# Kernel optimization log

Hardware: AMD Instinct MI355X
Metric: run time of the kernel (lower is better)

Reference implementation:

```python
import jax, jax.numpy as jnp
import numpy as np

CATS = [1000, 1000, 2000]
NDS = len(CATS)
TOT = sum(CATS)          # total_cats = 4000
N = TOT + NDS            # 4003 source (label) nodes
U = 2048                 # num_unify_class
NFEAT = 256
F = 256                  # nfeat_out
OUT_FEAT = 512           # output_feat_dim
ADJ_FEAT = 256           # adj_feat_dim
SINKHORN_ITERS = 20


def setup_inputs() -> dict:
    key = jax.random.key(0)
    ks = jax.random.split(key, 16)

    def rn(k, shape, s):
        return jax.random.normal(k, shape, dtype=jnp.float32) * s

    return {
        "datasets_node_features": jax.random.normal(ks[0], (TOT, NFEAT), dtype=jnp.float32),
        "unlable_node_features": rn(ks[1], (NDS, NFEAT), 0.02),  # trunc_normal_(std=0.02)
        "adj_matrix": jax.random.uniform(ks[2], (N, U), dtype=jnp.float32),  # torch.rand init
        "W_before": rn(ks[3], (NFEAT, F), 0.05), "b_before": jnp.zeros((F,), jnp.float32),
        "gc1_W": rn(ks[4], (F, F), 0.05), "gc1_b": jnp.zeros((F,), jnp.float32),
        "gc2_W": rn(ks[5], (F, F), 0.05), "gc2_b": jnp.zeros((F,), jnp.float32),
        "gc3_W": rn(ks[6], (F, F), 0.05), "gc3_b": jnp.zeros((F,), jnp.float32),
        "W1": rn(ks[7], (F, OUT_FEAT), 0.05), "b1": jnp.zeros((OUT_FEAT,), jnp.float32),
        "W2": rn(ks[8], (OUT_FEAT, ADJ_FEAT), 0.05), "b2": jnp.zeros((ADJ_FEAT,), jnp.float32),
    }


def _log_optimal_transport(scores, iters):
    # log-space Sinkhorn with uniform marginals 1/(m+n), then rescale by (m+n)
    m, n = scores.shape
    norm = -jnp.log(jnp.asarray(m + n, scores.dtype))
    log_mu = jnp.full((m,), norm, scores.dtype)
    log_nu = jnp.full((n,), norm, scores.dtype)

    def body(carry, _):
        u, v = carry
        u = log_mu - jax.nn.logsumexp(scores + v[None, :], axis=1)
        v = log_nu - jax.nn.logsumexp(scores + u[:, None], axis=0)
        return (u, v), None

    (u, v), _ = jax.lax.scan(body, (jnp.zeros_like(log_mu), jnp.zeros_like(log_nu)),
                             None, length=iters)
    return scores + u[:, None] + v[None, :] - norm


def reference(datasets_node_features, unlable_node_features, adj_matrix,
              W_before, b_before, gc1_W, gc1_b, gc2_W, gc2_b, gc3_W, gc3_b,
              W1, b1, W2, b2):
    # node features: dataset class nodes + per-dataset 'unlabeled' nodes -> [N, NFEAT]
    feats = jnp.concatenate([datasets_node_features, unlable_node_features], axis=0)
    x = jax.nn.relu(feats @ W_before + b_before)  # [N, F]

    # learnable adjacency normalized via differentiable Sinkhorn OT  [N, U]
    A = jnp.exp(_log_optimal_transport(adj_matrix, SINKHORN_ITERS))

    # bipartite message passing: full graph adj has zero diagonal blocks,
    # so spmm(adj, h) splits into A @ h_u (into label nodes) and A.T @ h_n (into unify nodes).
    hn = x                 # [N, F] label-node features
    hu = A.T @ x           # [U, F] initial unify-node features via aggregation

    def gcn(hn, hu, W, b):
        # GraphConvolution: spmm(adj, h @ W) + b ; GCN wrapper: tanh(out + h)
        new_n = jnp.tanh(A @ (hu @ W) + b + hn)
        new_u = jnp.tanh(A.T @ (hn @ W) + b + hu)
        return new_n, new_u

    hn, hu = gcn(hn, hu, gc1_W, gc1_b)
    hn, hu = gcn(hn, hu, gc2_W, gc2_b)
    hn, hu = gcn(hn, hu, gc3_W, gc3_b)

    # output head on unify nodes: linear1 -> relu -> linear2  [U, ADJ_FEAT]
    out = jax.nn.relu(hu @ W1 + b1) @ W2 + b2
    return out
```

## Files before the change

### kernel.cpp

```cpp
#include <hip/hip_runtime.h>
#include <hip/hip_fp16.h>
#include <math.h>

#define NN 4003
#define UU 2048
#define KP 4032
#define N4P 4004
#define NORMC (-8.7079796f)

using bf16x8 = __attribute__((ext_vector_type(8))) short;
using f32x4  = __attribute__((ext_vector_type(4))) float;

#define GLL16(g, l) __builtin_amdgcn_global_load_lds( \
    (const __attribute__((address_space(1))) unsigned*)(g), \
    (__attribute__((address_space(3))) unsigned*)(l), 16, 0, 0)

__device__ __forceinline__ ushort f2bf(float x) {
    unsigned u = __builtin_bit_cast(unsigned, x);
    u += 0x7fff + ((u >> 16) & 1);
    return (ushort)(u >> 16);
}
__device__ __forceinline__ float bf2f(ushort h) {
    unsigned u = ((unsigned)h) << 16;
    return __builtin_bit_cast(float, u);
}
__device__ __forceinline__ void bfsplit(float x, ushort& hi, ushort& lo) {
    hi = f2bf(x);
    lo = f2bf(x - bf2f(hi));
}
__device__ __forceinline__ float h2f(ushort h) {
    return __half2float(__ushort_as_half(h));
}

__global__ void concat_bf(const float* __restrict__ a, const float* __restrict__ b,
                          ushort* __restrict__ fh, ushort* __restrict__ fl,
                          float* __restrict__ u_ext, float* __restrict__ v) {
    int bid = blockIdx.x;
    if (bid >= 1001) {
        if (bid < 1003) {
            int t = (bid - 1001) * 256 + threadIdx.x;
            if (t < 512) ((float4*)v)[t] = (float4){0.f, 0.f, 0.f, 0.f};
        } else {
            if ((int)threadIdx.x < KP - NN) u_ext[NN + threadIdx.x] = -1e30f;
        }
        return;
    }
    int i = bid * 256 + threadIdx.x;
    const int tot4 = NN * 256 / 4;
    if (i >= tot4) return;
    float4 vv = (i < 256000) ? ((const float4*)a)[i] : ((const float4*)b)[i - 256000];
    ushort4 hv, lv;
    bfsplit(vv.x, hv.x, lv.x); bfsplit(vv.y, hv.y, lv.y);
    bfsplit(vv.z, hv.z, lv.z); bfsplit(vv.w, hv.w, lv.w);
    *(ushort4*)(fh + ((size_t)i << 2)) = hv;
    *(ushort4*)(fl + ((size_t)i << 2)) = lv;
}

__global__ void convW_all(
        const float* __restrict__ Wa, const float* __restrict__ Wb_,
        const float* __restrict__ Wc, const float* __restrict__ Wd,
        const float* __restrict__ We, const float* __restrict__ Wf,
        ushort* T0h, ushort* T0l, ushort* T1h, ushort* T1l,
        ushort* T2h, ushort* T2l, ushort* T3h, ushort* T3l,
        ushort* T4h, ushort* T4l, ushort* T5h, ushort* T5l) {
    __shared__ float tile[32][33];
    const float* W; ushort* Th; ushort* Tl; int K, Nw;
    switch (blockIdx.z) {
        case 0:  W = Wa;  Th = T0h; Tl = T0l; K = 256; Nw = 256; break;
        case 1:  W = Wb_; Th = T1h; Tl = T1l; K = 256; Nw = 256; break;
        case 2:  W = Wc;  Th = T2h; Tl = T2l; K = 256; Nw = 256; break;
        case 3:  W = Wd;  Th = T3h; Tl = T3l; K = 256; Nw = 256; break;
        case 4:  W = We;  Th = T4h; Tl = T4l; K = 256; Nw = 512; break;
        default: W = Wf;  Th = T5h; Tl = T5l; K = 512; Nw = 256; break;
    }
    int bx = blockIdx.x, by = blockIdx.y;
    if (bx * 32 >= Nw || by * 32 >= K) return;
    int tx = threadIdx.x;
    for (int r = threadIdx.y; r < 32; r += 8)
        tile[r][tx] = W[(size_t)(by * 32 + r) * Nw + bx * 32 + tx];
    __syncthreads();
    for (int r = threadIdx.y; r < 32; r += 8) {
        int n = bx * 32 + r, k = by * 32 + tx;
        ushort hi, lo; bfsplit(tile[tx][r], hi, lo);
        Th[(size_t)n * K + k] = hi;
        Tl[(size_t)n * K + k] = lo;
    }
}

__global__ void conv_both(const float* __restrict__ in, ushort* __restrict__ Sh,
                          ushort* __restrict__ STh) {
    __shared__ float tile[32][33];
    int x = blockIdx.x * 32 + threadIdx.x;
    int y0 = blockIdx.y * 32;
    for (int r = threadIdx.y; r < 32; r += 8) {
        int y = y0 + r;
        float vv = (y < NN) ? in[(size_t)y * UU + x] : 0.0f;
        tile[r][threadIdx.x] = vv;
        if (y < NN)
            Sh[(size_t)y * UU + x] = __half_as_ushort(__float2half(vv));
    }
    __syncthreads();
    int oc = y0 + threadIdx.x;
    for (int r = threadIdx.y; r < 32; r += 8) {
        int orow = blockIdx.x * 32 + r;
        STh[(size_t)orow * KP + oc] = __half_as_ushort(__float2half(tile[threadIdx.x][r]));
    }
}

__device__ __forceinline__ void wave_lse_reduce(float& m, float& s) {
    #pragma unroll
    for (int off = 1; off < 64; off <<= 1) {
        float om = __shfl_xor(m, off, 64), os = __shfl_xor(s, off, 64);
        float nm = fmaxf(m, om);
        s = s * __expf(m - nm) + os * __expf(om - nm);
        m = nm;
    }
}

__global__ __launch_bounds__(256) void lse4h(const ushort* __restrict__ Sh, int lda,
                                             const float* __restrict__ addv,
                                             float* __restrict__ outv, int C, int R) {
    int r0 = blockIdx.x * 4;
    const ushort* rp[4];
    #pragma unroll
    for (int q = 0; q < 4; ++q) {
        int r = r0 + q; if (r >= R) r = R - 1;
        rp[q] = Sh + (size_t)r * lda;
    }
    float m[4], s[4];
    #pragma unroll
    for (int q = 0; q < 4; ++q) { m[q] = -INFINITY; s[q] = 0.0f; }
    int C4 = C >> 2;
    for (int j = threadIdx.x; j < C4; j += 256) {
        float4 av = ((const float4*)addv)[j];
        #pragma unroll
        for (int q = 0; q < 4; ++q) {
            ushort4 pa = *(const ushort4*)(rp[q] + (j << 2));
            float x0 = h2f(pa.x) + av.x, x1 = h2f(pa.y) + av.y;
            float x2 = h2f(pa.z) + av.z, x3 = h2f(pa.w) + av.w;
            float mx = fmaxf(fmaxf(x0, x1), fmaxf(x2, x3));
            float nm = fmaxf(m[q], mx);
            s[q] = s[q] * __expf(m[q] - nm) + __expf(x0 - nm) + __expf(x1 - nm)
                                            + __expf(x2 - nm) + __expf(x3 - nm);
            m[q] = nm;
        }
    }
    int rem = C & 3;
    if ((int)threadIdx.x < rem) {
        int j = (C4 << 2) + threadIdx.x;
        float av = addv[j];
        #pragma unroll
        for (int q = 0; q < 4; ++q) {
            float x = h2f(rp[q][j]) + av;
            float nm = fmaxf(m[q], x);
            s[q] = s[q] * __expf(m[q] - nm) + __expf(x - nm);
            m[q] = nm;
        }
    }
    #pragma unroll
    for (int q = 0; q < 4; ++q) wave_lse_reduce(m[q], s[q]);
    __shared__ float sm[4][4], ss[4][4];
    int w = threadIdx.x >> 6;
    if ((threadIdx.x & 63) == 0) {
        #pragma unroll
        for (int q = 0; q < 4; ++q) { sm[w][q] = m[q]; ss[w][q] = s[q]; }
    }
    __syncthreads();
    if (threadIdx.x < 4) {
        int q = threadIdx.x;
        float mm = sm[0][q], sa = ss[0][q];
        #pragma unroll
        for (int i = 1; i < 4; ++i) {
            float om = sm[i][q], os = ss[i][q];
            float nm = fmaxf(mm, om);
            sa = sa * __expf(mm - nm) + os * __expf(om - nm);
            mm = nm;
        }
        int r = r0 + q;
        if (r < R) outv[r] = NORMC - (mm + __logf(sa));
    }
}

__device__ __forceinline__ void exp_row8h(const ushort* __restrict__ Sh,
        const float* __restrict__ rowadd, const float* __restrict__ coladd,
        int lda, int M, int gm, int kbase, uint4& hiv, uint4& lov) {
    ushort h[8], l[8];
    if (gm < M) {
        float ra = rowadd[gm] - NORMC;
        const ushort* rp = Sh + (size_t)gm * lda + kbase;
        ushort4 q0 = *(const ushort4*)rp;
        ushort4 q1 = *(const ushort4*)(rp + 4);
        float4 ca = *(const float4*)(coladd + kbase);
        float4 cb = *(const float4*)(coladd + kbase + 4);
        float vv[8] = {h2f(q0.x) + ca.x, h2f(q0.y) + ca.y, h2f(q0.z) + ca.z, h2f(q0.w) + ca.w,
                       h2f(q1.x) + cb.x, h2f(q1.y) + cb.y, h2f(q1.z) + cb.z, h2f(q1.w) + cb.w};
        #pragma unroll
        for (int e = 0; e < 8; ++e) {
            float av = __expf(vv[e] + ra);
            bfsplit(av, h[e], l[e]);
        }
    } else {
        #pragma unroll
        for (int e = 0; e < 8; ++e) { h[e] = 0; l[e] = 0; }
    }
    hiv.x = (unsigned)h[0] | ((unsigned)h[1] << 16);
    hiv.y = (unsigned)h[2] | ((unsigned)h[3] << 16);
    hiv.z = (unsigned)h[4] | ((unsigned)h[5] << 16);
    hiv.w = (unsigned)h[6] | ((unsigned)h[7] << 16);
    lov.x = (unsigned)l[0] | ((unsigned)l[1] << 16);
    lov.y = (unsigned)l[2] | ((unsigned)l[3] << 16);
    lov.z = (unsigned)l[4] | ((unsigned)l[5] << 16);
    lov.w = (unsigned)l[6] | ((unsigned)l[7] << 16);
}

__global__ __launch_bounds__(512) __attribute__((amdgpu_waves_per_eu(2, 4)))
void gemm_bigN(
        const ushort* __restrict__ Sh, const float* __restrict__ rowadd,
        const float* __restrict__ coladd, int lda,
        const ushort* __restrict__ Bh, const ushort* __restrict__ Bl, int ldb,
        float* __restrict__ P, int M, int K, int Kc) {
    __shared__ __align__(16) ushort SM[2 * 64 * 64 + 2 * 256 * 64];
    ushort* As0 = SM;
    ushort* As1 = SM + 4096;
    ushort* Bs0 = SM + 8192;
    ushort* Bs1 = SM + 8192 + 16384;
    const int tid = threadIdx.x;
    const int bm = blockIdx.x << 6;
    const int lane = tid & 63;
    const int wv = tid >> 6;
    const int wr = (wv >> 2) << 5;
    const int wc = (wv & 3) << 6;
    const int kb = blockIdx.y * Kc;
    int ke = kb + Kc; if (ke > K) ke = K;
    const int arow = tid >> 3, ak8 = (tid & 7) << 3;
    const int as = ((arow << 6) + ak8) ^ ((arow & 7) << 3);
    const int brow_base = wv << 5;
    f32x4 acc[2][4] = {};
    for (int k0 = kb; k0 < ke; k0 += 64) {
        uint4 ah, al;
        exp_row8h(Sh, rowadd, coladd, lda, M, bm + arow, k0 + ak8, ah, al);
        __syncthreads();
        #pragma unroll
        for (int t = 0; t < 4; ++t) {
            int rb2 = brow_base + (t << 3);
            int row = rb2 + (lane >> 3);
            int kksrc = (((lane & 7) ^ (row & 7)) << 3);
            size_t go = (size_t)row * ldb + k0 + kksrc;
            GLL16(Bh + go, &Bs0[rb2 << 6]);
            GLL16(Bl + go, &Bs1[rb2 << 6]);
        }
        *(uint4*)&As0[as] = ah;
        *(uint4*)&As1[as] = al;
        __syncthreads();
        #pragma unroll
        for (int ks = 0; ks < 2; ++ks) {
            int kq = (ks << 5) + ((lane >> 4) << 3);
            bf16x8 fah[2], fal[2], fbh[4], fbl[4];
            #pragma unroll
            for (int f = 0; f < 2; ++f) {
                int rr = wr + (f << 4) + (lane & 15);
                int ia = ((rr << 6) + kq) ^ ((rr & 7) << 3);
                fah[f] = *(const bf16x8*)&As0[ia];
                fal[f] = *(const bf16x8*)&As1[ia];
            }
            #pragma unroll
            for (int g = 0; g < 4; ++g) {
                int cc = wc + (g << 4) + (lane & 15);
                int ib = ((cc << 6) + kq) ^ ((cc & 7) << 3);
                fbh[g] = *(const bf16x8*)&Bs0[ib];
                fbl[g] = *(const bf16x8*)&Bs1[ib];
            }
            #pragma unroll
            for (int i = 0; i < 2; ++i)
                #pragma unroll
                for (int j = 0; j < 4; ++j) {
                    acc[i][j] = __builtin_amdgcn_mfma_f32_16x16x32_bf16(fah[i], fbh[j], acc[i][j], 0, 0, 0);
                    acc[i][j] = __builtin_amdgcn_mfma_f32_16x16x32_bf16(fah[i], fbl[j], acc[i][j], 0, 0, 0);
                    acc[i][j] = __builtin_amdgcn_mfma_f32_16x16x32_bf16(fal[i], fbh[j], acc[i][j], 0, 0, 0);
                }
        }
    }
    __syncthreads();
    float* LF = (float*)SM;
    #pragma unroll
    for (int i = 0; i < 2; ++i) {
        int row0 = wr + (i << 4) + ((lane >> 4) << 2);
        #pragma unroll
        for (int j = 0; j < 4; ++j) {
            int col = wc + (j << 4) + (lane & 15);
            #pragma unroll
            for (int r = 0; r < 4; ++r)
                LF[(row0 + r) * 256 + col] = acc[i][j][r];
        }
    }
    __syncthreads();
    float* Pp = P + (size_t)blockIdx.y * ((size_t)M * 256);
    #pragma unroll
    for (int it = 0; it < 8; ++it) {
        int idx = tid + (it << 9);
        int row = idx >> 6, c4 = (idx & 63) << 2;
        if (bm + row < M)
            *(float4*)(Pp + (size_t)(bm + row) * 256 + c4) = *(const float4*)&LF[row * 256 + c4];
    }
}

__global__ __launch_bounds__(256) __attribute__((amdgpu_waves_per_eu(4, 8)))
void gemm_ks(
        const ushort* __restrict__ Ah, const ushort* __restrict__ Al, int lda,
        const ushort* __restrict__ Bh, const ushort* __restrict__ Bl, int ldb, int Nb,
        float* __restrict__ P, int M, int Nplane, int K, int Kc) {
    __shared__ __align__(16) ushort SM[4 * 64 * 64];
    ushort* As0 = SM;
    ushort* As1 = SM + 4096;
    ushort* Bs0 = SM + 8192;
    ushort* Bs1 = SM + 12288;
    const int tid = threadIdx.x;
    const int bm = blockIdx.y << 6, bn = blockIdx.x << 6;
    const int lane = tid & 63;
    const int wv = tid >> 6;
    const int wm = (wv >> 1) << 5, wn = (wv & 1) << 5;
    const int kb = blockIdx.z * Kc;
    int ke = kb + Kc; if (ke > K) ke = K;
    const int rb = wv << 4;
    f32x4 acc[2][2] = {};
    for (int k0 = kb; k0 < ke; k0 += 64) {
        __syncthreads();
        #pragma unroll
        for (int t = 0; t < 2; ++t) {
            int rb2 = rb + (t << 3);
            int row = rb2 + (lane >> 3);
            int kksrc = (((lane & 7) ^ (row & 7)) << 3);
            int ga = bm + row; ga = (ga < M) ? ga : (M - 1);
            int gb = bn + row; gb = (gb < Nb) ? gb : (Nb - 1);
            size_t goa = (size_t)ga * lda + k0 + kksrc;
            size_t gob = (size_t)gb * ldb + k0 + kksrc;
            GLL16(Ah + goa, &As0[rb2 << 6]);
            GLL16(Al + goa, &As1[rb2 << 6]);
            GLL16(Bh + gob, &Bs0[rb2 << 6]);
            GLL16(Bl + gob, &Bs1[rb2 << 6]);
        }
        __syncthreads();
        #pragma unroll
        for (int ks = 0; ks < 2; ++ks) {
            int kbq = (ks << 5) + ((lane >> 4) << 3);
            bf16x8 fah[2], fal[2], fbh[2], fbl[2];
            #pragma unroll
            for (int f = 0; f < 2; ++f) {
                int rr = wm + (f << 4) + (lane & 15);
                int ia = ((rr << 6) + kbq) ^ ((rr & 7) << 3);
                fah[f] = *(const bf16x8*)&As0[ia];
                fal[f] = *(const bf16x8*)&As1[ia];
                int cc = wn + (f << 4) + (lane & 15);
                int ib = ((cc << 6) + kbq) ^ ((cc & 7) << 3);
                fbh[f] = *(const bf16x8*)&Bs0[ib];
                fbl[f] = *(const bf16x8*)&Bs1[ib];
            }
            #pragma unroll
            for (int i = 0; i < 2; ++i)
                #pragma unroll
                for (int j = 0; j < 2; ++j) {
                    acc[i][j] = __builtin_amdgcn_mfma_f32_16x16x32_bf16(fah[i], fbh[j], acc[i][j], 0, 0, 0);
                    acc[i][j] = __builtin_amdgcn_mfma_f32_16x16x32_bf16(fah[i], fbl[j], acc[i][j], 0, 0, 0);
                    acc[i][j] = __builtin_amdgcn_mfma_f32_16x16x32_bf16(fal[i], fbh[j], acc[i][j], 0, 0, 0);
                }
        }
    }
    __syncthreads();
    float* LF = (float*)SM;
    #pragma unroll
    for (int i = 0; i < 2; ++i) {
        int row0 = wm + (i << 4) + ((lane >> 4) << 2);
        #pragma unroll
        for (int j = 0; j < 2; ++j) {
            int col = wn + (j << 4) + (lane & 15);
            #pragma unroll
            for (int r = 0; r < 4; ++r)
                LF[(row0 + r) * 64 + col] = acc[i][j][r];
        }
    }
    __syncthreads();
    float* Pp = P + (size_t)blockIdx.z * ((size_t)M * Nplane);
    #pragma unroll
    for (int it = 0; it < 4; ++it) {
        int idx = tid + (it << 8);
        int row = idx >> 4, c4 = (idx & 15) << 2;
        if (bm + row < M && bn + c4 < Nplane)
            *(float4*)(Pp + (size_t)(bm + row) * Nplane + bn + c4) = *(const float4*)&LF[row * 64 + c4];
    }
}

template<int ACT, int BIAS, int RES, int OUTK>
__global__ __launch_bounds__(256) void reduce_ks(
        const float* __restrict__ P, int zg,
        const float* __restrict__ bias,
        const ushort* __restrict__ Rh, const ushort* __restrict__ Rl,
        float* __restrict__ Cf, ushort* __restrict__ Ch, ushort* __restrict__ Cl,
        int M, int N4, int ldo) {
    int t = blockIdx.x * 256 + threadIdx.x;
    int n4w = N4 >> 2;
    int tot = M * n4w;
    if (t >= tot) return;
    int m = t / n4w;
    int n = (t - m * n4w) << 2;
    size_t pstr = (size_t)M * N4;
    const float* base = P + (size_t)m * N4 + n;
    float4 a = *(const float4*)base;
    for (int z = 1; z < zg; ++z) {
        float4 b = *(const float4*)(base + (size_t)z * pstr);
        a.x += b.x; a.y += b.y; a.z += b.z; a.w += b.w;
    }
    if (BIAS == 1) {
        float4 bv = *(const float4*)(bias + n);
        a.x += bv.x; a.y += bv.y; a.z += bv.z; a.w += bv.w;
    }
    if (BIAS == 2) {
        float s = bias[m];
        a.x += s; a.y += s; a.z += s; a.w += s;
    }
    if (RES) {
        size_t ro = (size_t)m * ldo + n;
        ushort4 rh = *(const ushort4*)(Rh + ro);
        ushort4 rl = *(const ushort4*)(Rl + ro);
        a.x += bf2f(rh.x) + bf2f(rl.x); a.y += bf2f(rh.y) + bf2f(rl.y);
        a.z += bf2f(rh.z) + bf2f(rl.z); a.w += bf2f(rh.w) + bf2f(rl.w);
    }
    if (ACT == 1) {
        a.x = fmaxf(a.x, 0.f); a.y = fmaxf(a.y, 0.f);
        a.z = fmaxf(a.z, 0.f); a.w = fmaxf(a.w, 0.f);
    }
    if (ACT == 2) {
        a.x = tanhf(a.x); a.y = tanhf(a.y); a.z = tanhf(a.z); a.w = tanhf(a.w);
    }
    size_t co = (size_t)m * ldo + n;
    if (OUTK == 0) {
        *(float4*)(Cf + co) = a;
    } else {
        ushort4 hv, lv;
        bfsplit(a.x, hv.x, lv.x); bfsplit(a.y, hv.y, lv.y);
        bfsplit(a.z, hv.z, lv.z); bfsplit(a.w, hv.w, lv.w);
        *(ushort4*)(Ch + co) = hv;
        *(ushort4*)(Cl + co) = lv;
    }
}

static inline int rgrid(int M, int N4) { return (M * (N4 >> 2) + 255) / 256; }

extern "C" void kernel_launch(void* const* d_in, const int* in_sizes, int n_in,
                              void* d_out, int out_size, void* d_ws, size_t ws_size,
                              hipStream_t stream) {
    const float* dsf = (const float*)d_in[0];
    const float* unl = (const float*)d_in[1];
    const float* S   = (const float*)d_in[2];
    const float* Wb  = (const float*)d_in[3];
    const float* bb  = (const float*)d_in[4];
    const float* gcW[3] = {(const float*)d_in[5], (const float*)d_in[7], (const float*)d_in[9]};
    const float* gcb[3] = {(const float*)d_in[6], (const float*)d_in[8], (const float*)d_in[10]};
    const float* W1 = (const float*)d_in[11];
    const float* b1 = (const float*)d_in[12];
    const float* W2 = (const float*)d_in[13];
    const float* b2 = (const float*)d_in[14];
    float* out = (float*)d_out;

    char* p = (char*)d_ws;
    ushort* Shm = (ushort*)p; p += (size_t)NN * UU * 2;
    ushort* STh = (ushort*)p; p += (size_t)UU * KP * 2;
    float* P    = (float*)p;  p += (size_t)8 * NN * 256 * 4;
    ushort* fh = (ushort*)p; ushort* fl = fh + (size_t)NN * 256; p += (size_t)NN * 256 * 4;
    ushort* xh = (ushort*)p; ushort* xl = xh + (size_t)NN * 256; p += (size_t)NN * 256 * 4;
    ushort* xTh = (ushort*)p; ushort* xTl = xTh + (size_t)256 * KP; p += (size_t)256 * KP * 4;
    ushort* huh = (ushort*)p; ushort* hul = huh + (size_t)UU * 256; p += (size_t)UU * 256 * 4;
    ushort* tuTh = (ushort*)p; ushort* tuTl = tuTh + (size_t)256 * UU; p += (size_t)256 * UU * 4;
    ushort* tnTh = (ushort*)p; ushort* tnTl = tnTh + (size_t)256 * KP; p += (size_t)256 * KP * 4;
    float* u_ext = (float*)p; p += KP * 4;
    float* v     = (float*)p; p += UU * 4;
    ushort* WbTh = (ushort*)p; ushort* WbTl = WbTh + 256 * 256; p += 256 * 256 * 4;
    ushort* gWh[3]; ushort* gWl[3];
    for (int l = 0; l < 3; ++l) { gWh[l] = (ushort*)p; gWl[l] = gWh[l] + 256 * 256; p += 256 * 256 * 4; }
    ushort* W1Th = (ushort*)p; ushort* W1Tl = W1Th + 512 * 256; p += 512 * 256 * 4;
    ushort* W2Th = (ushort*)p; ushort* W2Tl = W2Th + 256 * 512; p += 256 * 512 * 4;
    ushort* h1h = xh; ushort* h1l = h1h + (size_t)UU * 512;
    (void)ws_size;

    concat_bf<<<dim3(1004), dim3(256), 0, stream>>>(dsf, unl, fh, fl, u_ext, v);
    convW_all<<<dim3(16, 16, 6), dim3(32, 8), 0, stream>>>(
        Wb, gcW[0], gcW[1], gcW[2], W1, W2,
        WbTh, WbTl, gWh[0], gWl[0], gWh[1], gWl[1], gWh[2], gWl[2],
        W1Th, W1Tl, W2Th, W2Tl);
    conv_both<<<dim3(64, 126), dim3(32, 8), 0, stream>>>(S, Shm, STh);

    gemm_ks<<<dim3(4, 63, 2), 256, 0, stream>>>(
        fh, fl, 256, WbTh, WbTl, 256, 256, P, NN, 256, 256, 128);
    reduce_ks<1,1,0,1><<<rgrid(NN,256), 256, 0, stream>>>(
        P, 2, bb, nullptr, nullptr, nullptr, xh, xl, NN, 256, 256);
    gemm_ks<<<dim3(63, 4, 2), 256, 0, stream>>>(
        WbTh, WbTl, 256, fh, fl, 256, NN, P, 256, N4P, 256, 128);
    reduce_ks<1,2,0,1><<<rgrid(256,N4P), 256, 0, stream>>>(
        P, 2, bb, nullptr, nullptr, nullptr, xTh, xTl, 256, N4P, KP);

    for (int it = 0; it < 20; ++it) {
        lse4h<<<dim3((NN + 3) / 4), dim3(256), 0, stream>>>(Shm, UU, v, u_ext, UU, NN);
        lse4h<<<dim3(UU / 4),       dim3(256), 0, stream>>>(STh, KP, u_ext, v, NN, UU);
    }

    gemm_bigN<<<dim3(32, 8), 512, 0, stream>>>(
        STh, v, u_ext, KP, xTh, xTl, KP, P, UU, KP, 512);
    reduce_ks<0,0,0,1><<<rgrid(UU,256), 256, 0, stream>>>(
        P, 8, nullptr, nullptr, nullptr, nullptr, huh, hul, UU, 256, 256);

    for (int l = 0; l < 3; ++l) {
        const ushort* hnh = (l == 0) ? xh : fh;
        const ushort* hnl = (l == 0) ? xl : fl;
        if (l < 2) {
            gemm_ks<<<dim3(32, 4, 2), 256, 0, stream>>>(
                gWh[l], gWl[l], 256, huh, hul, 256, UU, P, 256, UU, 256, 128);
            reduce_ks<0,0,0,1><<<rgrid(256,UU), 256, 0, stream>>>(
                P, 2, nullptr, nullptr, nullptr, nullptr, tuTh, tuTl, 256, UU, UU);
        }
        gemm_ks<<<dim3(63, 4, 2), 256, 0, stream>>>(
            gWh[l], gWl[l], 256, hnh, hnl, 256, NN, P, 256, N4P, 256, 128);
        reduce_ks<0,0,0,1><<<rgrid(256,N4P), 256, 0, stream>>>(
            P, 2, nullptr, nullptr, nullptr, nullptr, tnTh, tnTl, 256, N4P, KP);
        if (l < 2) {
            gemm_bigN<<<dim3(63, 6), 512, 0, stream>>>(
                Shm, u_ext, v, UU, tuTh, tuTl, UU, P, NN, UU, 384);
            reduce_ks<2,1,1,1><<<rgrid(NN,256), 256, 0, stream>>>(
                P, 6, gcb[l], hnh, hnl, nullptr, fh, fl, NN, 256, 256);
        }
        gemm_bigN<<<dim3(32, 8), 512, 0, stream>>>(
            STh, v, u_ext, KP, tnTh, tnTl, KP, P, UU, KP, 512);
        reduce_ks<2,1,1,1><<<rgrid(UU,256), 256, 0, stream>>>(
            P, 8, gcb[l], huh, hul, nullptr, huh, hul, UU, 256, 256);
    }

    gemm_ks<<<dim3(8, 32, 2), 256, 0, stream>>>(
        huh, hul, 256, W1Th, W1Tl, 256, 512, P, UU, 512, 256, 128);
    reduce_ks<1,1,0,1><<<rgrid(UU,512), 256, 0, stream>>>(
        P, 2, b1, nullptr, nullptr, nullptr, h1h, h1l, UU, 512, 512);
    gemm_ks<<<dim3(4, 32, 4), 256, 0, stream>>>(
        h1h, h1l, 512, W2Th, W2Tl, 512, 256, P, UU, 256, 512, 128);
    reduce_ks<0,1,0,0><<<rgrid(UU,256), 256, 0, stream>>>(
        P, 4, b2, nullptr, nullptr, out, nullptr, nullptr, UU, 256, 256);
}
```

Before: 560.2 us.

## Fuse split-K reductions into GEMM kernels via last-block atomic counters

Removes the separate reduce_ks launches. Each split-K GEMM block now writes its partial tile, fences, and bumps a per-tile atomic counter. The last block for a tile sums all partials and applies bias, residual, activation and the bf16 hi/lo split itself. Counters are zeroed in concat_bf. This cuts about 14 kernel launches and their gaps, at the cost of atomics, fences and one serial reduction block per tile.

```diff
diff --git a/kernel.cpp b/kernel.cpp
--- a/kernel.cpp
+++ b/kernel.cpp
@@ -34,14 +34,18 @@
 
 __global__ void concat_bf(const float* __restrict__ a, const float* __restrict__ b,
                           ushort* __restrict__ fh, ushort* __restrict__ fl,
-                          float* __restrict__ u_ext, float* __restrict__ v) {
+                          float* __restrict__ u_ext, float* __restrict__ v,
+                          int* __restrict__ ctr) {
     int bid = blockIdx.x;
     if (bid >= 1001) {
         if (bid < 1003) {
             int t = (bid - 1001) * 256 + threadIdx.x;
             if (t < 512) ((float4*)v)[t] = (float4){0.f, 0.f, 0.f, 0.f};
+        } else if (bid == 1003) {
+            if ((int)threadIdx.x < KP - NN) u_ext[NN + threadIdx.x] = -1e30f;
         } else {
-            if ((int)threadIdx.x < KP - NN) u_ext[NN + threadIdx.x] = -1e30f;
+            int t = (bid - 1004) * 256 + threadIdx.x;
+            if (t < 960) ((int4*)ctr)[t] = (int4){0, 0, 0, 0};
         }
         return;
     }
@@ -213,12 +217,17 @@
     lov.w = (unsigned)l[6] | ((unsigned)l[7] << 16);
 }
 
+template<int ACT, int BIAS, int RES>
 __global__ __launch_bounds__(512) __attribute__((amdgpu_waves_per_eu(2, 4)))
 void gemm_bigN(
         const ushort* __restrict__ Sh, const float* __restrict__ rowadd,
         const float* __restrict__ coladd, int lda,
         const ushort* __restrict__ Bh, const ushort* __restrict__ Bl, int ldb,
-        float* __restrict__ P, int M, int K, int Kc) {
+        float* __restrict__ P, int M, int K, int Kc,
+        const float* __restrict__ bias,
+        const ushort* __restrict__ Rh, const ushort* __restrict__ Rl,
+        ushort* __restrict__ Ch, ushort* __restrict__ Cl,
+        int* __restrict__ ctr) {
     __shared__ __align__(16) ushort SM[2 * 64 * 64 + 2 * 256 * 64];
     ushort* As0 = SM;
     ushort* As1 = SM + 4096;
@@ -302,13 +311,58 @@
         if (bm + row < M)
             *(float4*)(Pp + (size_t)(bm + row) * 256 + c4) = *(const float4*)&LF[row * 256 + c4];
     }
-}
-
+    __threadfence();
+    __shared__ int lastf;
+    if (tid == 0) lastf = (atomicAdd(ctr + blockIdx.x, 1) == (int)gridDim.y - 1);
+    __syncthreads();
+    if (!lastf) return;
+    __threadfence();
+    const int zg = gridDim.y;
+    const size_t pstr = (size_t)M * 256;
+    #pragma unroll
+    for (int it = 0; it < 8; ++it) {
+        int idx = tid + (it << 9);
+        int row = idx >> 6, c4 = (idx & 63) << 2;
+        int grow = bm + row;
+        if (grow >= M) continue;
+        const float* base = P + (size_t)grow * 256 + c4;
+        float4 a = *(const float4*)base;
+        for (int z = 1; z < zg; ++z) {
+            float4 b2 = *(const float4*)(base + (size_t)z * pstr);
+            a.x += b2.x; a.y += b2.y; a.z += b2.z; a.w += b2.w;
+        }
+        if (BIAS == 1) {
+            float4 bv = *(const float4*)(bias + c4);
+            a.x += bv.x; a.y += bv.y; a.z += bv.z; a.w += bv.w;
+        }
+        if (RES) {
+            size_t ro = (size_t)grow * 256 + c4;
+            ushort4 rh = *(const ushort4*)(Rh + ro);
+            ushort4 rl = *(const ushort4*)(Rl + ro);
+            a.x += bf2f(rh.x) + bf2f(rl.x); a.y += bf2f(rh.y) + bf2f(rl.y);
+            a.z += bf2f(rh.z) + bf2f(rl.z); a.w += bf2f(rh.w) + bf2f(rl.w);
+        }
+        if (ACT == 2) {
+            a.x = tanhf(a.x); a.y = tanhf(a.y); a.z = tanhf(a.z); a.w = tanhf(a.w);
+        }
+        ushort4 hv, lv;
+        bfsplit(a.x, hv.x, lv.x); bfsplit(a.y, hv.y, lv.y);
+        bfsplit(a.z, hv.z, lv.z); bfsplit(a.w, hv.w, lv.w);
+        size_t co = (size_t)grow * 256 + c4;
+        *(ushort4*)(Ch + co) = hv;
+        *(ushort4*)(Cl + co) = lv;
+    }
+}
+
+template<int ACT, int BIAS, int OUTF>
 __global__ __launch_bounds__(256) __attribute__((amdgpu_waves_per_eu(4, 8)))
 void gemm_ks(
         const ushort* __restrict__ Ah, const ushort* __restrict__ Al, int lda,
         const ushort* __restrict__ Bh, const ushort* __restrict__ Bl, int ldb, int Nb,
-        float* __restrict__ P, int M, int Nplane, int K, int Kc) {
+        float* __restrict__ P, int M, int Nplane, int K, int Kc,
+        const float* __restrict__ bias,
+        float* __restrict__ Cf, ushort* __restrict__ Ch, ushort* __restrict__ Cl,
+        int ldo, int* __restrict__ ctr) {
     __shared__ __align__(16) ushort SM[4 * 64 * 64];
     ushort* As0 = SM;
     ushort* As1 = SM + 4096;
@@ -387,63 +441,51 @@
         if (bm + row < M && bn + c4 < Nplane)
             *(float4*)(Pp + (size_t)(bm + row) * Nplane + bn + c4) = *(const float4*)&LF[row * 64 + c4];
     }
-}
-
-template<int ACT, int BIAS, int RES, int OUTK>
-__global__ __launch_bounds__(256) void reduce_ks(
-        const float* __restrict__ P, int zg,
-        const float* __restrict__ bias,
-        const ushort* __restrict__ Rh, const ushort* __restrict__ Rl,
-        float* __restrict__ Cf, ushort* __restrict__ Ch, ushort* __restrict__ Cl,
-        int M, int N4, int ldo) {
-    int t = blockIdx.x * 256 + threadIdx.x;
-    int n4w = N4 >> 2;
-    int tot = M * n4w;
-    if (t >= tot) return;
-    int m = t / n4w;
-    int n = (t - m * n4w) << 2;
-    size_t pstr = (size_t)M * N4;
-    const float* base = P + (size_t)m * N4 + n;
-    float4 a = *(const float4*)base;
-    for (int z = 1; z < zg; ++z) {
-        float4 b = *(const float4*)(base + (size_t)z * pstr);
-        a.x += b.x; a.y += b.y; a.z += b.z; a.w += b.w;
-    }
-    if (BIAS == 1) {
-        float4 bv = *(const float4*)(bias + n);
-        a.x += bv.x; a.y += bv.y; a.z += bv.z; a.w += bv.w;
-    }
-    if (BIAS == 2) {
-        float s = bias[m];
-        a.x += s; a.y += s; a.z += s; a.w += s;
-    }
-    if (RES) {
-        size_t ro = (size_t)m * ldo + n;
-        ushort4 rh = *(const ushort4*)(Rh + ro);
-        ushort4 rl = *(const ushort4*)(Rl + ro);
-        a.x += bf2f(rh.x) + bf2f(rl.x); a.y += bf2f(rh.y) + bf2f(rl.y);
-        a.z += bf2f(rh.z) + bf2f(rl.z); a.w += bf2f(rh.w) + bf2f(rl.w);
-    }
-    if (ACT == 1) {
-        a.x = fmaxf(a.x, 0.f); a.y = fmaxf(a.y, 0.f);
-        a.z = fmaxf(a.z, 0.f); a.w = fmaxf(a.w, 0.f);
-    }
-    if (ACT == 2) {
-        a.x = tanhf(a.x); a.y = tanhf(a.y); a.z = tanhf(a.z); a.w = tanhf(a.w);
-    }
-    size_t co = (size_t)m * ldo + n;
-    if (OUTK == 0) {
-        *(float4*)(Cf + co) = a;
-    } else {
-        ushort4 hv, lv;
-        bfsplit(a.x, hv.x, lv.x); bfsplit(a.y, hv.y, lv.y);
-        bfsplit(a.z, hv.z, lv.z); bfsplit(a.w, hv.w, lv.w);
-        *(ushort4*)(Ch + co) = hv;
-        *(ushort4*)(Cl + co) = lv;
-    }
-}
-
-static inline int rgrid(int M, int N4) { return (M * (N4 >> 2) + 255) / 256; }
+    __threadfence();
+    __shared__ int lastf;
+    if (tid == 0)
+        lastf = (atomicAdd(ctr + blockIdx.y * gridDim.x + blockIdx.x, 1) == (int)gridDim.z - 1);
+    __syncthreads();
+    if (!lastf) return;
+    __threadfence();
+    const int zg = gridDim.z;
+    const size_t pstr = (size_t)M * Nplane;
+    #pragma unroll
+    for (int it = 0; it < 16; ++it) {
+        int idx = tid + (it << 8);
+        int row = idx >> 4, c4 = (idx & 15) << 2;
+        int grow = bm + row, gcol = bn + c4;
+        if (grow >= M || gcol >= Nplane) continue;
+        const float* base = P + (size_t)grow * Nplane + gcol;
+        float4 a = *(const float4*)base;
+        for (int z = 1; z < zg; ++z) {
+            float4 b2 = *(const float4*)(base + (size_t)z * pstr);
+            a.x += b2.x; a.y += b2.y; a.z += b2.z; a.w += b2.w;
+        }
+        if (BIAS == 1) {
+            float4 bv = *(const float4*)(bias + gcol);
+            a.x += bv.x; a.y += bv.y; a.z += bv.z; a.w += bv.w;
+        }
+        if (BIAS == 2) {
+            float sb = bias[grow];
+            a.x += sb; a.y += sb; a.z += sb; a.w += sb;
+        }
+        if (ACT == 1) {
+            a.x = fmaxf(a.x, 0.f); a.y = fmaxf(a.y, 0.f);
+            a.z = fmaxf(a.z, 0.f); a.w = fmaxf(a.w, 0.f);
+        }
+        size_t co = (size_t)grow * ldo + gcol;
+        if (OUTF) {
+            *(float4*)(Cf + co) = a;
+        } else {
+            ushort4 hv, lv;
+            bfsplit(a.x, hv.x, lv.x); bfsplit(a.y, hv.y, lv.y);
+            bfsplit(a.z, hv.z, lv.z); bfsplit(a.w, hv.w, lv.w);
+            *(ushort4*)(Ch + co) = hv;
+            *(ushort4*)(Cl + co) = lv;
+        }
+    }
+}
 
 extern "C" void kernel_launch(void* const* d_in, const int* in_sizes, int n_in,
                               void* d_out, int out_size, void* d_ws, size_t ws_size,
@@ -478,66 +520,59 @@
     for (int l = 0; l < 3; ++l) { gWh[l] = (ushort*)p; gWl[l] = gWh[l] + 256 * 256; p += 256 * 256 * 4; }
     ushort* W1Th = (ushort*)p; ushort* W1Tl = W1Th + 512 * 256; p += 512 * 256 * 4;
     ushort* W2Th = (ushort*)p; ushort* W2Tl = W2Th + 256 * 512; p += 256 * 512 * 4;
+    int* CTR = (int*)p; p += 15 * 256 * 4;
     ushort* h1h = xh; ushort* h1l = h1h + (size_t)UU * 512;
     (void)ws_size;
-
-    concat_bf<<<dim3(1004), dim3(256), 0, stream>>>(dsf, unl, fh, fl, u_ext, v);
+    int ci = 0;
+
+    concat_bf<<<dim3(1008), dim3(256), 0, stream>>>(dsf, unl, fh, fl, u_ext, v, CTR);
     convW_all<<<dim3(16, 16, 6), dim3(32, 8), 0, stream>>>(
         Wb, gcW[0], gcW[1], gcW[2], W1, W2,
         WbTh, WbTl, gWh[0], gWl[0], gWh[1], gWl[1], gWh[2], gWl[2],
         W1Th, W1Tl, W2Th, W2Tl);
     conv_both<<<dim3(64, 126), dim3(32, 8), 0, stream>>>(S, Shm, STh);
 
-    gemm_ks<<<dim3(4, 63, 2), 256, 0, stream>>>(
-        fh, fl, 256, WbTh, WbTl, 256, 256, P, NN, 256, 256, 128);
-    reduce_ks<1,1,0,1><<<rgrid(NN,256), 256, 0, stream>>>(
-        P, 2, bb, nullptr, nullptr, nullptr, xh, xl, NN, 256, 256);
-    gemm_ks<<<dim3(63, 4, 2), 256, 0, stream>>>(
-        WbTh, WbTl, 256, fh, fl, 256, NN, P, 256, N4P, 256, 128);
-    reduce_ks<1,2,0,1><<<rgrid(256,N4P), 256, 0, stream>>>(
-        P, 2, bb, nullptr, nullptr, nullptr, xTh, xTl, 256, N4P, KP);
+    gemm_ks<1,1,0><<<dim3(4, 63, 2), 256, 0, stream>>>(
+        fh, fl, 256, WbTh, WbTl, 256, 256, P, NN, 256, 256, 128,
+        bb, nullptr, xh, xl, 256, CTR + 256 * ci); ci++;
+    gemm_ks<1,2,0><<<dim3(63, 4, 2), 256, 0, stream>>>(
+        WbTh, WbTl, 256, fh, fl, 256, NN, P, 256, N4P, 256, 128,
+        bb, nullptr, xTh, xTl, KP, CTR + 256 * ci); ci++;
 
     for (int it = 0; it < 20; ++it) {
         lse4h<<<dim3((NN + 3) / 4), dim3(256), 0, stream>>>(Shm, UU, v, u_ext, UU, NN);
         lse4h<<<dim3(UU / 4),       dim3(256), 0, stream>>>(STh, KP, u_ext, v, NN, UU);
     }
 
-    gemm_bigN<<<dim3(32, 8), 512, 0, stream>>>(
-        STh, v, u_ext, KP, xTh, xTl, KP, P, UU, KP, 512);
-    reduce_ks<0,0,0,1><<<rgrid(UU,256), 256, 0, stream>>>(
-        P, 8, nullptr, nullptr, nullptr, nullptr, huh, hul, UU, 256, 256);
+    gemm_bigN<0,0,0><<<dim3(32, 8), 512, 0, stream>>>(
+        STh, v, u_ext, KP, xTh, xTl, KP, P, UU, KP, 512,
+        nullptr, nullptr, nullptr, huh, hul, CTR + 256 * ci); ci++;
 
     for (int l = 0; l < 3; ++l) {
         const ushort* hnh = (l == 0) ? xh : fh;
         const ushort* hnl = (l == 0) ? xl : fl;
         if (l < 2) {
-            gemm_ks<<<dim3(32, 4, 2), 256, 0, stream>>>(
-                gWh[l], gWl[l], 256, huh, hul, 256, UU, P, 256, UU, 256, 128);
-            reduce_ks<0,0,0,1><<<rgrid(256,UU), 256, 0, stream>>>(
-                P, 2, nullptr, nullptr, nullptr, nullptr, tuTh, tuTl, 256, UU, UU);
-        }
-        gemm_ks<<<dim3(63, 4, 2), 256, 0, stream>>>(
-            gWh[l], gWl[l], 256, hnh, hnl, 256, NN, P, 256, N4P, 256, 128);
-        reduce_ks<0,0,0,1><<<rgrid(256,N4P), 256, 0, stream>>>(
-            P, 2, nullptr, nullptr, nullptr, nullptr, tnTh, tnTl, 256, N4P, KP);
+            gemm_ks<0,0,0><<<dim3(32, 4, 2), 256, 0, stream>>>(
+                gWh[l], gWl[l], 256, huh, hul, 256, UU, P, 256, UU, 256, 128,
+                nullptr, nullptr, tuTh, tuTl, UU, CTR + 256 * ci); ci++;
+        }
+        gemm_ks<0,0,0><<<dim3(63, 4, 2), 256, 0, stream>>>(
+            gWh[l], gWl[l], 256, hnh, hnl, 256, NN, P, 256, N4P, 256, 128,
+            nullptr, nullptr, tnTh, tnTl, KP, CTR + 256 * ci); ci++;
         if (l < 2) {
-            gemm_bigN<<<dim3(63, 6), 512, 0, stream>>>(
-                Shm, u_ext, v, UU, tuTh, tuTl, UU, P, NN, UU, 384);
-            reduce_ks<2,1,1,1><<<rgrid(NN,256), 256, 0, stream>>>(
-                P, 6, gcb[l], hnh, hnl, nullptr, fh, fl, NN, 256, 256);
-        }
-        gemm_bigN<<<dim3(32, 8), 512, 0, stream>>>(
-            STh, v, u_ext, KP, tnTh, tnTl, KP, P, UU, KP, 512);
-        reduce_ks<2,1,1,1><<<rgrid(UU,256), 256, 0, stream>>>(
-            P, 8, gcb[l], huh, hul, nullptr, huh, hul, UU, 256, 256);
-    }
-
-    gemm_ks<<<dim3(8, 32, 2), 256, 0, stream>>>(
-        huh, hul, 256, W1Th, W1Tl, 256, 512, P, UU, 512, 256, 128);
-    reduce_ks<1,1,0,1><<<rgrid(UU,512), 256, 0, stream>>>(
-        P, 2, b1, nullptr, nullptr, nullptr, h1h, h1l, UU, 512, 512);
-    gemm_ks<<<dim3(4, 32, 4), 256, 0, stream>>>(
-        h1h, h1l, 512, W2Th, W2Tl, 512, 256, P, UU, 256, 512, 128);
-    reduce_ks<0,1,0,0><<<rgrid(UU,256), 256, 0, stream>>>(
-        P, 4, b2, nullptr, nullptr, out, nullptr, nullptr, UU, 256, 256);
-}
+            gemm_bigN<2,1,1><<<dim3(63, 6), 512, 0, stream>>>(
+                Shm, u_ext, v, UU, tuTh, tuTl, UU, P, NN, UU, 384,
+                gcb[l], hnh, hnl, fh, fl, CTR + 256 * ci); ci++;
+        }
+        gemm_bigN<2,1,1><<<dim3(32, 8), 512, 0, stream>>>(
+            STh, v, u_ext, KP, tnTh, tnTl, KP, P, UU, KP, 512,
+            gcb[l], huh, hul, huh, hul, CTR + 256 * ci); ci++;
+    }
+
+    gemm_ks<1,1,0><<<dim3(8, 32, 2), 256, 0, stream>>>(
+        huh, hul, 256, W1Th, W1Tl, 256, 512, P, UU, 512, 256, 128,
+        b1, nullptr, h1h, h1l, 512, CTR + 256 * ci); ci++;
+    gemm_ks<0,1,1><<<dim3(4, 32, 4), 256, 0, stream>>>(
+        h1h, h1l, 512, W2Th, W2Tl, 512, 256, P, UU, 256, 512, 128,
+        b2, out, nullptr, nullptr, 256, CTR + 256 * ci); ci++;
+}
```

Result: slower. 1.730 ms (+208.8%).
